# Optimization experiments

Hardware: AMD Instinct MI355X
Metric: run time of the kernel (lower is better)

Reference implementation:

```python
import jax, jax.numpy as jnp
import numpy as np

N, E, G = 20000, 160000, 32          # nodes, edges, graphs in batch
F_IN, H, P, C = 67, 2048, 1024, 18   # in_feat, hidden_feat, fc2 width, n_classifier
EPS = 1e-5
SLOPE = 0.01  # leaky_relu default negative slope


def setup_inputs() -> dict:
    key = jax.random.key(0)
    ks = jax.random.split(key, 24)
    w = lambda k, shape: (jax.random.normal(k, shape, jnp.float32) * 0.02)
    return {
        "h": jax.random.normal(ks[0], (N, F_IN), jnp.float32),
        "src": jax.random.randint(ks[1], (E,), 0, N),
        "dst": jax.random.randint(ks[2], (E,), 0, N),
        "gids": jnp.sort(jax.random.randint(ks[3], (N,), 0, G)),
        # SAGEConv layers: fc_self, fc_neigh (no per-fc bias), shared bias
        "ws1": w(ks[4], (F_IN, H)), "wn1": w(ks[5], (F_IN, H)), "b1": jnp.zeros((H,), jnp.float32),
        "ws2": w(ks[6], (H, H)),    "wn2": w(ks[7], (H, H)),    "b2": jnp.zeros((H,), jnp.float32),
        "ws3": w(ks[8], (H, H)),    "wn3": w(ks[9], (H, H)),    "b3": jnp.zeros((H,), jnp.float32),
        # batch norms (gamma, beta)
        "g1": jnp.ones((H,), jnp.float32), "be1": jnp.zeros((H,), jnp.float32),
        "g2": jnp.ones((H,), jnp.float32), "be2": jnp.zeros((H,), jnp.float32),
        "g3": jnp.ones((H,), jnp.float32), "be3": jnp.zeros((H,), jnp.float32),
        # MLP head
        "fw1": w(ks[10], (H, H)), "fb1": jnp.zeros((H,), jnp.float32),
        "fw2": w(ks[11], (H, P)), "fb2": jnp.zeros((P,), jnp.float32),
        "fw3": w(ks[12], (P, C)), "fb3": jnp.zeros((C,), jnp.float32),
    }


def _leaky(x):
    return jnp.where(x >= 0, x, SLOPE * x)


def _sage(x, src, dst, w_self, w_neigh, b):
    # DGL SAGEConv 'mean': mean of neighbor (src) features into dst, then linears.
    nsum = jax.ops.segment_sum(x[src], dst, num_segments=N)            # [N, F]
    deg = jax.ops.segment_sum(jnp.ones((E,), x.dtype), dst, num_segments=N)
    neigh = nsum / jnp.maximum(deg, 1.0)[:, None]                      # 0 for isolated
    return x @ w_self + neigh @ w_neigh + b


def _bn(x, gamma, beta):
    m = x.mean(0)
    v = x.var(0)
    return (x - m) * jax.lax.rsqrt(v + EPS) * gamma + beta


def reference(h, src, dst, gids,
              ws1, wn1, b1, g1, be1,
              ws2, wn2, b2, g2, be2,
              ws3, wn3, b3, g3, be3,
              fw1, fb1, fw2, fb2, fw3, fb3):
    x = _leaky(_bn(_sage(h, src, dst, ws1, wn1, b1), g1, be1))
    x = _leaky(_bn(_sage(x, src, dst, ws2, wn2, b2), g2, be2))
    x = _leaky(_bn(_sage(x, src, dst, ws3, wn3, b3), g3, be3))
    # mean pooling per graph
    gsum = jax.ops.segment_sum(x, gids, num_segments=G)                # [G, H]
    cnt = jax.ops.segment_sum(jnp.ones((N,), x.dtype), gids, num_segments=G)
    hg = gsum / jnp.maximum(cnt, 1.0)[:, None]
    # dropouts are identity in eval
    y = _leaky(hg @ fw1 + fb1)
    y = _leaky(y @ fw2 + fb2)
    return y @ fw3 + fb3
```

## Files before the change

### kernel.cpp

```cpp
#include <hip/hip_runtime.h>

typedef unsigned short u16;
typedef __attribute__((ext_vector_type(4))) float f32x4;
typedef __attribute__((ext_vector_type(8))) __bf16 bf16x8;
typedef __attribute__((ext_vector_type(8))) short s16x8;
typedef __attribute__((ext_vector_type(4))) u16 u16x4;

#define N_NODES 20000
#define N_EDGES 160000
#define N_GRAPH 32
#define F_IN 67
#define HID 2048
#define PW 1024
#define NCLS 18
#define MPAD2 20224
#define K1 192

__device__ __forceinline__ float bf2f(u16 u) {
    unsigned v = ((unsigned)u) << 16;
    float f; __builtin_memcpy(&f, &v, 4); return f;
}
__device__ __forceinline__ u16 f2bf(float f) {
    unsigned u; __builtin_memcpy(&u, &f, 4);
    u = (u + 0x7FFF + ((u >> 16) & 1)) >> 16;
    return (u16)u;
}
__device__ __forceinline__ int imax(int a, int b) { return a > b ? a : b; }

__device__ __forceinline__ void ld16(const u16* gptr, u16* lptr) {
    __builtin_amdgcn_global_load_lds(
        (const __attribute__((address_space(1))) unsigned int*)gptr,
        (__attribute__((address_space(3))) unsigned int*)lptr,
        16, 0, 0);
}

__global__ void k_hist(const int* __restrict__ dst, int* __restrict__ cnt) {
    int e = blockIdx.x * 256 + threadIdx.x;
    if (e < N_EDGES) atomicAdd(&cnt[dst[e]], 1);
}

__global__ void k_scan(const int* __restrict__ cnt, int* __restrict__ rowptr) {
    __shared__ int part[256];
    int t = threadIdx.x;
    const int per = (N_NODES + 255) / 256;
    int base = t * per;
    int s = 0;
    for (int i = 0; i < per; i++) { int idx = base + i; if (idx < N_NODES) s += cnt[idx]; }
    part[t] = s; __syncthreads();
    for (int off = 1; off < 256; off <<= 1) {
        int v = (t >= off) ? part[t - off] : 0;
        __syncthreads();
        part[t] += v;
        __syncthreads();
    }
    int running = (t == 0) ? 0 : part[t - 1];
    for (int i = 0; i < per; i++) {
        int idx = base + i;
        if (idx < N_NODES) { rowptr[idx] = running; running += cnt[idx]; }
    }
    if (t == 255) rowptr[N_NODES] = running;
}

__global__ void k_scatter(const int* __restrict__ src, const int* __restrict__ dst,
                          const int* __restrict__ rowptr, int* __restrict__ cursor,
                          int* __restrict__ csr) {
    int e = blockIdx.x * 256 + threadIdx.x;
    if (e < N_EDGES) {
        int d = dst[e];
        int p = atomicAdd(&cursor[d], 1);
        csr[rowptr[d] + p] = src[e];
    }
}

__global__ void k_w1t(const float* __restrict__ ws1, const float* __restrict__ wn1,
                      u16* __restrict__ w1t) {
    int n = blockIdx.x, t = threadIdx.x;
    float v = 0.f;
    if (t < F_IN) v = ws1[(size_t)t * HID + n];
    else if (t < 2 * F_IN) v = wn1[(size_t)(t - F_IN) * HID + n];
    w1t[(size_t)n * K1 + t] = f2bf(v);
}

__global__ void k_transpose2(const float* __restrict__ s0, const float* __restrict__ s1,
                             u16* __restrict__ dst) {
    __shared__ float tile[32][33];
    const float* src = blockIdx.z ? s1 : s0;
    int colofs = blockIdx.z ? HID : 0;
    int bx = blockIdx.x * 32, by = blockIdx.y * 32;
    int tx = threadIdx.x, ty = threadIdx.y;
#pragma unroll
    for (int i = 0; i < 32; i += 8)
        tile[ty + i][tx] = src[(size_t)(by + ty + i) * HID + bx + tx];
    __syncthreads();
#pragma unroll
    for (int i = 0; i < 32; i += 8)
        dst[(size_t)(bx + ty + i) * (2 * HID) + colofs + by + tx] = f2bf(tile[tx][ty + i]);
}

__global__ void k_agg1(const float* __restrict__ h, const int* __restrict__ rowptr,
                       const int* __restrict__ csr, u16* __restrict__ acat) {
    int n = blockIdx.x, t = threadIdx.x;
    if (t < F_IN) {
        acat[(size_t)n * K1 + t] = f2bf(h[(size_t)n * F_IN + t]);
    } else if (t < 2 * F_IN) {
        int c = t - F_IN;
        int e0 = rowptr[n], e1 = rowptr[n + 1];
        float a = 0.f;
        for (int e = e0; e < e1; e++) a += h[(size_t)csr[e] * F_IN + c];
        acat[(size_t)n * K1 + F_IN + c] = f2bf(a / (float)imax(e1 - e0, 1));
    }
}

__global__ __launch_bounds__(256)
void k_agg(const u16* __restrict__ x, const int* __restrict__ rowptr,
           const int* __restrict__ csr, u16* __restrict__ out) {
    int n = blockIdx.x, t = threadIdx.x;
    int e0 = rowptr[n], e1 = rowptr[n + 1];
    float acc[8] = {0, 0, 0, 0, 0, 0, 0, 0};
    for (int e = e0; e < e1; e++) {
        int s = csr[e];
        s16x8 v = *(const s16x8*)&x[(size_t)s * HID + t * 8];
#pragma unroll
        for (int j = 0; j < 8; j++) acc[j] += bf2f((u16)v[j]);
    }
    float inv = 1.0f / (float)imax(e1 - e0, 1);
    s16x8 o;
#pragma unroll
    for (int j = 0; j < 8; j++) o[j] = (short)f2bf(acc[j] * inv);
    *(s16x8*)&out[(size_t)n * HID + t * 8] = o;
}

#define VM4 asm volatile("s_waitcnt vmcnt(4)" ::: "memory")
#define VM2 asm volatile("s_waitcnt vmcnt(2)" ::: "memory")
#define VM0 asm volatile("s_waitcnt vmcnt(0)" ::: "memory")

#define STAGE_A(H) { const u16* as_; int ktl_;                                      \
    if (kt1 < kskt) { as_ = A0; ktl_ = kt1; } else { as_ = A1; ktl_ = kt1 - kskt; } \
    size_t ko_ = (size_t)ktl_ * 64 + swe;                                           \
    ld16(as_ + (row0 + 0 * 128 + (H) * 64 + r8) * (size_t)lda + ko_,                \
         LA + dbo + ((H) * 128 + 0 * 64 + r8) * 64 + ld8);                          \
    ld16(as_ + (row0 + 1 * 128 + (H) * 64 + r8) * (size_t)lda + ko_,                \
         LA + dbo + ((H) * 128 + 1 * 64 + r8) * 64 + ld8); }

#define STAGE_B(H) { size_t ko_ = (size_t)kt1 * 64 + swe;                           \
    ld16(WT + ((size_t)col0 + ((r8 >> 5)) * 64 + (H) * 32 + (r8 & 31)) * (size_t)ldb + ko_,\
         LB + dbo + ((H) * 128 + 0 * 64 + r8) * 64 + ld8);                          \
    ld16(WT + ((size_t)col0 + (2 + (r8 >> 5)) * 64 + (H) * 32 + (r8 & 31)) * (size_t)ldb + ko_,\
         LB + dbo + ((H) * 128 + 1 * 64 + r8) * 64 + ld8); }

#define RD_A(QM) {                                                                  \
    _Pragma("unroll") for (int f = 0; f < 4; ++f)                                   \
      _Pragma("unroll") for (int kk = 0; kk < 2; ++kk)                              \
        af[f][kk] = *(const bf16x8*)(bA + (QM) * 16384 + (wm * 64 + f * 16 + lr) * 128 \
                                     + ((kk * 64 + lg * 16) ^ rxor)); }

#define RD_B(DST, QN) {                                                             \
    _Pragma("unroll") for (int n = 0; n < 2; ++n)                                   \
      _Pragma("unroll") for (int kk = 0; kk < 2; ++kk)                              \
        DST[n][kk] = *(const bf16x8*)(bB + (QN) * 16384 + (wn * 32 + n * 16 + lr) * 128 \
                                     + ((kk * 64 + lg * 16) ^ rxor)); }

#define SYNC_MM(QM, QN, BW) {                                                       \
    __builtin_amdgcn_s_barrier();                                                   \
    __builtin_amdgcn_s_setprio(1);                                                  \
    _Pragma("unroll") for (int kk = 0; kk < 2; ++kk)                                \
      _Pragma("unroll") for (int f = 0; f < 4; ++f)                                 \
        _Pragma("unroll") for (int n = 0; n < 2; ++n)                               \
          acc[(QM) * 4 + f][(QN) * 2 + n] = __builtin_amdgcn_mfma_f32_16x16x32_bf16(\
              BW[n][kk], af[f][kk], acc[(QM) * 4 + f][(QN) * 2 + n], 0, 0, 0);      \
    __builtin_amdgcn_s_setprio(0); }

__global__ __launch_bounds__(512, 2)
void k_gemm256(const u16* __restrict__ A0, const u16* __restrict__ A1,
               const u16* __restrict__ WT, u16* __restrict__ C,
               float* __restrict__ ssum, float* __restrict__ ssq,
               int nkt, int kskt, int lda, int ldb) {
    __shared__ u16 LA[2 * 256 * 64];
    __shared__ u16 LB[2 * 256 * 64];
    const int tid = threadIdx.x;
    const int lane = tid & 63;
    const int wave = tid >> 6;
    const int wm = wave >> 2, wn = wave & 3;
    const int lr = lane & 15, lg = lane >> 4;
    const int rxor = (lr & 7) << 4;

    const int g = (blockIdx.x & 7) * 79 + (blockIdx.x >> 3);
    const size_t row0 = (size_t)(g >> 3) * 256;
    const int col0 = (g & 7) * 256;

    const int r8 = tid >> 3;
    const int ld8 = (tid & 7) * 8;
    const int swe = ((ld8 * 2) ^ ((r8 & 7) << 4)) >> 1;

    f32x4 acc[8][4];
#pragma unroll
    for (int i = 0; i < 8; i++)
#pragma unroll
        for (int j = 0; j < 4; j++) acc[i][j] = f32x4{0.f, 0.f, 0.f, 0.f};

    {
        const int kt1 = 0; const int dbo = 0;
        STAGE_A(0) STAGE_B(0) STAGE_B(1) STAGE_A(1)
    }
    VM0;
    __builtin_amdgcn_s_barrier();

    bf16x8 af[4][2], bw[2][2], bw2[2][2];

    for (int t = 0; t < nkt - 1; ++t) {
        const char* bA = (const char*)LA + (t & 1) * 32768;
        const char* bB = (const char*)LB + (t & 1) * 32768;
        const int kt1 = t + 1;
        const int dbo = ((t + 1) & 1) * 16384;
        RD_A(0) RD_B(bw, 0) STAGE_A(0) VM4; SYNC_MM(0, 0, bw)
        RD_B(bw2, 1) STAGE_B(0) VM4; SYNC_MM(0, 1, bw2)
        RD_A(1) STAGE_B(1) SYNC_MM(1, 1, bw2)
        RD_B(bw, 0) STAGE_A(1) VM4; SYNC_MM(1, 0, bw)
    }
    {
        const char* bA = (const char*)LA + ((nkt - 1) & 1) * 32768;
        const char* bB = (const char*)LB + ((nkt - 1) & 1) * 32768;
        RD_A(0) RD_B(bw, 0) VM2; SYNC_MM(0, 0, bw)
        RD_B(bw2, 1) VM0; SYNC_MM(0, 1, bw2)
        RD_A(1) SYNC_MM(1, 1, bw2)
        RD_B(bw, 0) SYNC_MM(1, 0, bw)
    }

#pragma unroll
    for (int f = 0; f < 8; ++f) {
        size_t m = row0 + wm * 128 + f * 16 + lr;
#pragma unroll
        for (int n = 0; n < 4; ++n) {
            int cb = col0 + wn * 64 + n * 16 + lg * 4;
            u16x4 o;
#pragma unroll
            for (int rg = 0; rg < 4; ++rg) o[rg] = f2bf(acc[f][n][rg]);
            *(u16x4*)&C[m * HID + cb] = o;
        }
    }
#pragma unroll
    for (int n = 0; n < 4; ++n) {
#pragma unroll
        for (int rg = 0; rg < 4; ++rg) {
            float s = 0.f, s2 = 0.f;
#pragma unroll
            for (int f = 0; f < 8; ++f) { float v = acc[f][n][rg]; s += v; s2 += v * v; }
#pragma unroll
            for (int mk = 1; mk < 16; mk <<= 1) {
                s += __shfl_xor(s, mk, 64);
                s2 += __shfl_xor(s2, mk, 64);
            }
            if (lr == 0) {
                int cb = col0 + wn * 64 + n * 16 + lg * 4 + rg;
                atomicAdd(&ssum[cb], s);
                atomicAdd(&ssq[cb], s2);
            }
        }
    }
}

__global__ void k_bnleaky(const u16* __restrict__ xin,
                          const float* __restrict__ ssum, const float* __restrict__ ssq,
                          const float* __restrict__ gma, const float* __restrict__ bta,
                          u16* __restrict__ xout) {
    size_t eb = ((size_t)blockIdx.x * 256 + threadIdx.x) * 8;
    int col = (int)(eb & (HID - 1));
    s16x8 v = *(const s16x8*)&xin[eb];
    s16x8 o;
#pragma unroll
    for (int hq = 0; hq < 2; ++hq) {
        f32x4 su = *(const f32x4*)&ssum[col + hq * 4];
        f32x4 sq = *(const f32x4*)&ssq[col + hq * 4];
        f32x4 gm = *(const f32x4*)&gma[col + hq * 4];
        f32x4 bt = *(const f32x4*)&bta[col + hq * 4];
#pragma unroll
        for (int j = 0; j < 4; ++j) {
            float m = su[j] * (1.0f / N_NODES);
            float var = sq[j] * (1.0f / N_NODES) - m * m;
            float a = gm[j] * rsqrtf(var + 1e-5f);
            float d = bt[j] - m * a;
            float f = bf2f((u16)v[hq * 4 + j]) * a + d;
            f = f > 0.f ? f : 0.01f * f;
            o[hq * 4 + j] = (short)f2bf(f);
        }
    }
    *(s16x8*)&xout[eb] = o;
}

__global__ void k_bounds(const int* __restrict__ gids, int* __restrict__ gstart) {
    int t = threadIdx.x;
    if (t > N_GRAPH) return;
    int lo = 0, hi = N_NODES;
    while (lo < hi) { int mid = (lo + hi) >> 1; if (gids[mid] < t) lo = mid + 1; else hi = mid; }
    gstart[t] = lo;
}

__global__ void k_pool(const u16* __restrict__ x, const int* __restrict__ gstart,
                       float* __restrict__ hg) {
    int g = blockIdx.x;
    int col = blockIdx.y * 256 + threadIdx.x;
    int r0 = gstart[g], r1 = gstart[g + 1];
    float s = 0.f;
    for (int r = r0; r < r1; r++) s += bf2f(x[(size_t)r * HID + col]);
    hg[(size_t)g * HID + col] = s / (float)imax(r1 - r0, 1);
}

__global__ __launch_bounds__(256)
void k_mlp_part(const float* __restrict__ X, const float* __restrict__ W,
                float* __restrict__ Yp, int K, int Nc) {
    __shared__ float xs[32 * 256];
    int t = threadIdx.x;
    int kc = blockIdx.y;
    int n = blockIdx.x * 64 + (t & 63);
    int mg = t >> 6;
#pragma unroll
    for (int l = 0; l < 32; ++l) {
        int e = l * 256 + t;
        xs[e] = X[(size_t)(e >> 8) * K + kc * 256 + (e & 255)];
    }
    __syncthreads();
    float acc[8] = {};
    for (int k = 0; k < 256; ++k) {
        float wv = W[(size_t)(kc * 256 + k) * Nc + n];
#pragma unroll
        for (int i = 0; i < 8; ++i) acc[i] += xs[(mg * 8 + i) * 256 + k] * wv;
    }
#pragma unroll
    for (int i = 0; i < 8; ++i)
        Yp[(size_t)(kc * 32 + mg * 8 + i) * Nc + n] = acc[i];
}

__global__ void k_mlp_red(const float* __restrict__ Yp, const float* __restrict__ bias,
                          float* __restrict__ Y, int Nc, int leaky) {
    int idx = blockIdx.x * 256 + threadIdx.x;
    int n = idx % Nc;
    float s = 0.f;
#pragma unroll
    for (int kc = 0; kc < 8; ++kc) s += Yp[(size_t)kc * 32 * Nc + idx];
    float v = s + bias[n];
    if (leaky) v = v > 0.f ? v : 0.01f * v;
    Y[idx] = v;
}

__global__ void k_fc3(const float* __restrict__ y2, const float* __restrict__ fw3,
                      const float* __restrict__ fb3, float* __restrict__ out) {
    __shared__ float red[8][32];
    int m = blockIdx.x, t = threadIdx.x;
    int ch = t >> 5, c = t & 31;
    float s = 0.f;
    if (c < NCLS) {
        for (int j = 0; j < 128; ++j) {
            int k = ch * 128 + j;
            s += y2[(size_t)m * PW + k] * fw3[(size_t)k * NCLS + c];
        }
    }
    red[ch][c] = s;
    __syncthreads();
    if (t < NCLS) {
        float a = 0.f;
#pragma unroll
        for (int c2 = 0; c2 < 8; ++c2) a += red[c2][t];
        out[m * NCLS + t] = a + fb3[t];
    }
}

extern "C" void kernel_launch(void* const* d_in, const int* in_sizes, int n_in,
                              void* d_out, int out_size, void* d_ws, size_t ws_size,
                              hipStream_t stream) {
    const float* h   = (const float*)d_in[0];
    const int* src   = (const int*)d_in[1];
    const int* dst   = (const int*)d_in[2];
    const int* gids  = (const int*)d_in[3];
    const float* ws1 = (const float*)d_in[4];
    const float* wn1 = (const float*)d_in[5];
    const float* ws2 = (const float*)d_in[7];
    const float* wn2 = (const float*)d_in[8];
    const float* ws3 = (const float*)d_in[10];
    const float* wn3 = (const float*)d_in[11];
    const float* g1  = (const float*)d_in[13];
    const float* be1 = (const float*)d_in[14];
    const float* g2  = (const float*)d_in[15];
    const float* be2 = (const float*)d_in[16];
    const float* g3  = (const float*)d_in[17];
    const float* be3 = (const float*)d_in[18];
    const float* fw1 = (const float*)d_in[19];
    const float* fb1 = (const float*)d_in[20];
    const float* fw2 = (const float*)d_in[21];
    const float* fb2 = (const float*)d_in[22];
    const float* fw3 = (const float*)d_in[23];
    const float* fb3 = (const float*)d_in[24];
    float* out = (float*)d_out;
    (void)in_sizes; (void)n_in; (void)out_size;

    char* base = (char*)d_ws;
    size_t off = 0;
    auto alloc = [&](size_t b) -> char* {
        char* p = base + off;
        off += (b + 255) & ~(size_t)255;
        return p;
    };
    u16* BUF0 = (u16*)alloc((size_t)MPAD2 * HID * 2);
    u16* BUF1 = (u16*)alloc((size_t)MPAD2 * HID * 2);
    u16* BUF2 = (u16*)alloc((size_t)MPAD2 * HID * 2);
    u16* WT   = (u16*)alloc((size_t)HID * 2 * HID * 2);
    int* cnt    = (int*)alloc(N_NODES * 4);
    int* rowptr = (int*)alloc((N_NODES + 1) * 4);
    int* cursor = (int*)alloc(N_NODES * 4);
    int* csr    = (int*)alloc(N_EDGES * 4);
    float* ssum = (float*)alloc(HID * 4);
    float* ssq  = (float*)alloc(HID * 4);
    int* gstart = (int*)alloc(64 * 4);
    float* hg = (float*)alloc((size_t)N_GRAPH * HID * 4);
    float* y1 = (float*)alloc((size_t)N_GRAPH * HID * 4);
    float* y2 = (float*)alloc((size_t)N_GRAPH * PW * 4);
    u16* ACAT = (u16*)((char*)BUF2);
    u16* W1T  = (u16*)((char*)BUF2 + (size_t)MPAD2 * K1 * 2);
    float* Yp = (float*)((char*)BUF2);

    if (off > ws_size) return;

    hipMemsetAsync(cnt, 0, N_NODES * 4, stream);
    hipMemsetAsync(cursor, 0, N_NODES * 4, stream);
    hipMemsetAsync(ACAT, 0, (size_t)MPAD2 * K1 * 2, stream);
    hipMemsetAsync(BUF1 + (size_t)N_NODES * HID, 0, (size_t)(MPAD2 - N_NODES) * HID * 2, stream);
    hipMemsetAsync(BUF2 + (size_t)N_NODES * HID, 0, (size_t)(MPAD2 - N_NODES) * HID * 2, stream);

    k_hist<<<(N_EDGES + 255) / 256, 256, 0, stream>>>(dst, cnt);
    k_scan<<<1, 256, 0, stream>>>(cnt, rowptr);
    k_scatter<<<(N_EDGES + 255) / 256, 256, 0, stream>>>(src, dst, rowptr, cursor, csr);

    k_w1t<<<HID, K1, 0, stream>>>(ws1, wn1, W1T);
    k_agg1<<<N_NODES, 192, 0, stream>>>(h, rowptr, csr, ACAT);

    dim3 tb(32, 8);
    hipMemsetAsync(ssum, 0, 2 * HID * 4, stream);
    k_gemm256<<<632, 512, 0, stream>>>(ACAT, ACAT, W1T, BUF0, ssum, ssq, 3, 3, K1, K1);
    k_bnleaky<<<20000, 256, 0, stream>>>(BUF0, ssum, ssq, g1, be1, BUF1);
    k_transpose2<<<dim3(64, 64, 2), tb, 0, stream>>>(ws2, wn2, WT);
    k_agg<<<N_NODES, 256, 0, stream>>>(BUF1, rowptr, csr, BUF2);
    hipMemsetAsync(ssum, 0, 2 * HID * 4, stream);
    k_gemm256<<<632, 512, 0, stream>>>(BUF1, BUF2, WT, BUF0, ssum, ssq, 64, 32, HID, 2 * HID);
    k_bnleaky<<<20000, 256, 0, stream>>>(BUF0, ssum, ssq, g2, be2, BUF1);
    k_transpose2<<<dim3(64, 64, 2), tb, 0, stream>>>(ws3, wn3, WT);
    k_agg<<<N_NODES, 256, 0, stream>>>(BUF1, rowptr, csr, BUF2);
    hipMemsetAsync(ssum, 0, 2 * HID * 4, stream);
    k_gemm256<<<632, 512, 0, stream>>>(BUF1, BUF2, WT, BUF0, ssum, ssq, 64, 32, HID, 2 * HID);
    k_bnleaky<<<20000, 256, 0, stream>>>(BUF0, ssum, ssq, g3, be3, BUF1);
    k_bounds<<<1, 64, 0, stream>>>(gids, gstart);
    k_pool<<<dim3(N_GRAPH, HID / 256), 256, 0, stream>>>(BUF1, gstart, hg);
    k_mlp_part<<<dim3(HID / 64, 8), 256, 0, stream>>>(hg, fw1, Yp, HID, HID);
    k_mlp_red<<<(N_GRAPH * HID) / 256, 256, 0, stream>>>(Yp, fb1, y1, HID, 1);
    k_mlp_part<<<dim3(PW / 64, 8), 256, 0, stream>>>(y1, fw2, Yp, HID, PW);
    k_mlp_red<<<(N_GRAPH * PW) / 256, 256, 0, stream>>>(Yp, fb2, y2, PW, 1);
    k_fc3<<<N_GRAPH, 256, 0, stream>>>(y2, fw3, fb3, out);
}
```

Before: 1.408 ms.

## Fuse batchnorm+leaky into neighbor aggregation and graph pooling kernels

The separate batchnorm+leaky-relu pass is removed. BN affine and leaky are now applied on the fly inside the aggregation kernel, which writes both the normalized self features and the neighbor mean, and inside the pooling kernel for the last layer. This saves a full read+write pass over the 20000x2048 bf16 activation per layer and the final BN output write. In exchange, BN math is recomputed for every gathered neighbor row, and the pooled values use unrounded fp32 activations instead of bf16-rounded ones.

```diff
diff --git a/kernel.cpp b/kernel.cpp
--- a/kernel.cpp
+++ b/kernel.cpp
@@ -112,22 +112,46 @@
 }
 
 __global__ __launch_bounds__(256)
-void k_agg(const u16* __restrict__ x, const int* __restrict__ rowptr,
-           const int* __restrict__ csr, u16* __restrict__ out) {
+void k_aggbn(const u16* __restrict__ x,
+             const float* __restrict__ ssum, const float* __restrict__ ssq,
+             const float* __restrict__ gma, const float* __restrict__ bta,
+             const int* __restrict__ rowptr, const int* __restrict__ csr,
+             u16* __restrict__ self_out, u16* __restrict__ neigh_out) {
     int n = blockIdx.x, t = threadIdx.x;
+    int col = t * 8;
+    float a[8], d[8];
+#pragma unroll
+    for (int j = 0; j < 8; ++j) {
+        float m = ssum[col + j] * (1.0f / N_NODES);
+        float var = ssq[col + j] * (1.0f / N_NODES) - m * m;
+        a[j] = gma[col + j] * rsqrtf(var + 1e-5f);
+        d[j] = bta[col + j] - m * a[j];
+    }
+    s16x8 vs = *(const s16x8*)&x[(size_t)n * HID + col];
+    s16x8 so;
+#pragma unroll
+    for (int j = 0; j < 8; ++j) {
+        float f = bf2f((u16)vs[j]) * a[j] + d[j];
+        f = fmaxf(f, 0.01f * f);
+        so[j] = (short)f2bf(f);
+    }
+    *(s16x8*)&self_out[(size_t)n * HID + col] = so;
     int e0 = rowptr[n], e1 = rowptr[n + 1];
     float acc[8] = {0, 0, 0, 0, 0, 0, 0, 0};
-    for (int e = e0; e < e1; e++) {
+    for (int e = e0; e < e1; ++e) {
         int s = csr[e];
-        s16x8 v = *(const s16x8*)&x[(size_t)s * HID + t * 8];
-#pragma unroll
-        for (int j = 0; j < 8; j++) acc[j] += bf2f((u16)v[j]);
+        s16x8 v = *(const s16x8*)&x[(size_t)s * HID + col];
+#pragma unroll
+        for (int j = 0; j < 8; ++j) {
+            float f = bf2f((u16)v[j]) * a[j] + d[j];
+            acc[j] += fmaxf(f, 0.01f * f);
+        }
     }
     float inv = 1.0f / (float)imax(e1 - e0, 1);
     s16x8 o;
 #pragma unroll
-    for (int j = 0; j < 8; j++) o[j] = (short)f2bf(acc[j] * inv);
-    *(s16x8*)&out[(size_t)n * HID + t * 8] = o;
+    for (int j = 0; j < 8; ++j) o[j] = (short)f2bf(acc[j] * inv);
+    *(s16x8*)&neigh_out[(size_t)n * HID + col] = o;
 }
 
 #define VM4 asm volatile("s_waitcnt vmcnt(4)" ::: "memory")
@@ -259,34 +283,6 @@
     }
 }
 
-__global__ void k_bnleaky(const u16* __restrict__ xin,
-                          const float* __restrict__ ssum, const float* __restrict__ ssq,
-                          const float* __restrict__ gma, const float* __restrict__ bta,
-                          u16* __restrict__ xout) {
-    size_t eb = ((size_t)blockIdx.x * 256 + threadIdx.x) * 8;
-    int col = (int)(eb & (HID - 1));
-    s16x8 v = *(const s16x8*)&xin[eb];
-    s16x8 o;
-#pragma unroll
-    for (int hq = 0; hq < 2; ++hq) {
-        f32x4 su = *(const f32x4*)&ssum[col + hq * 4];
-        f32x4 sq = *(const f32x4*)&ssq[col + hq * 4];
-        f32x4 gm = *(const f32x4*)&gma[col + hq * 4];
-        f32x4 bt = *(const f32x4*)&bta[col + hq * 4];
-#pragma unroll
-        for (int j = 0; j < 4; ++j) {
-            float m = su[j] * (1.0f / N_NODES);
-            float var = sq[j] * (1.0f / N_NODES) - m * m;
-            float a = gm[j] * rsqrtf(var + 1e-5f);
-            float d = bt[j] - m * a;
-            float f = bf2f((u16)v[hq * 4 + j]) * a + d;
-            f = f > 0.f ? f : 0.01f * f;
-            o[hq * 4 + j] = (short)f2bf(f);
-        }
-    }
-    *(s16x8*)&xout[eb] = o;
-}
-
 __global__ void k_bounds(const int* __restrict__ gids, int* __restrict__ gstart) {
     int t = threadIdx.x;
     if (t > N_GRAPH) return;
@@ -295,13 +291,22 @@
     gstart[t] = lo;
 }
 
-__global__ void k_pool(const u16* __restrict__ x, const int* __restrict__ gstart,
-                       float* __restrict__ hg) {
+__global__ void k_poolbn(const u16* __restrict__ x,
+                         const float* __restrict__ ssum, const float* __restrict__ ssq,
+                         const float* __restrict__ gma, const float* __restrict__ bta,
+                         const int* __restrict__ gstart, float* __restrict__ hg) {
     int g = blockIdx.x;
     int col = blockIdx.y * 256 + threadIdx.x;
+    float m = ssum[col] * (1.0f / N_NODES);
+    float var = ssq[col] * (1.0f / N_NODES) - m * m;
+    float a = gma[col] * rsqrtf(var + 1e-5f);
+    float d = bta[col] - m * a;
     int r0 = gstart[g], r1 = gstart[g + 1];
     float s = 0.f;
-    for (int r = r0; r < r1; r++) s += bf2f(x[(size_t)r * HID + col]);
+    for (int r = r0; r < r1; r++) {
+        float f = bf2f(x[(size_t)r * HID + col]) * a + d;
+        s += fmaxf(f, 0.01f * f);
+    }
     hg[(size_t)g * HID + col] = s / (float)imax(r1 - r0, 1);
 }
 
@@ -435,19 +440,16 @@
     dim3 tb(32, 8);
     hipMemsetAsync(ssum, 0, 2 * HID * 4, stream);
     k_gemm256<<<632, 512, 0, stream>>>(ACAT, ACAT, W1T, BUF0, ssum, ssq, 3, 3, K1, K1);
-    k_bnleaky<<<20000, 256, 0, stream>>>(BUF0, ssum, ssq, g1, be1, BUF1);
+    k_aggbn<<<N_NODES, 256, 0, stream>>>(BUF0, ssum, ssq, g1, be1, rowptr, csr, BUF1, BUF2);
     k_transpose2<<<dim3(64, 64, 2), tb, 0, stream>>>(ws2, wn2, WT);
-    k_agg<<<N_NODES, 256, 0, stream>>>(BUF1, rowptr, csr, BUF2);
     hipMemsetAsync(ssum, 0, 2 * HID * 4, stream);
     k_gemm256<<<632, 512, 0, stream>>>(BUF1, BUF2, WT, BUF0, ssum, ssq, 64, 32, HID, 2 * HID);
-    k_bnleaky<<<20000, 256, 0, stream>>>(BUF0, ssum, ssq, g2, be2, BUF1);
+    k_aggbn<<<N_NODES, 256, 0, stream>>>(BUF0, ssum, ssq, g2, be2, rowptr, csr, BUF1, BUF2);
     k_transpose2<<<dim3(64, 64, 2), tb, 0, stream>>>(ws3, wn3, WT);
-    k_agg<<<N_NODES, 256, 0, stream>>>(BUF1, rowptr, csr, BUF2);
     hipMemsetAsync(ssum, 0, 2 * HID * 4, stream);
     k_gemm256<<<632, 512, 0, stream>>>(BUF1, BUF2, WT, BUF0, ssum, ssq, 64, 32, HID, 2 * HID);
-    k_bnleaky<<<20000, 256, 0, stream>>>(BUF0, ssum, ssq, g3, be3, BUF1);
     k_bounds<<<1, 64, 0, stream>>>(gids, gstart);
-    k_pool<<<dim3(N_GRAPH, HID / 256), 256, 0, stream>>>(BUF1, gstart, hg);
+    k_poolbn<<<dim3(N_GRAPH, HID / 256), 256, 0, stream>>>(BUF0, ssum, ssq, g3, be3, gstart, hg);
     k_mlp_part<<<dim3(HID / 64, 8), 256, 0, stream>>>(hg, fw1, Yp, HID, HID);
     k_mlp_red<<<(N_GRAPH * HID) / 256, 256, 0, stream>>>(Yp, fb1, y1, HID, 1);
     k_mlp_part<<<dim3(PW / 64, 8), 256, 0, stream>>>(y1, fw2, Yp, HID, PW);
```

Result: faster. 1.351 ms (median of 2 runs) (-4.0%).
